# Kernel optimization log

Hardware: AMD Instinct MI355X
Metric: run time of the kernel (lower is better)

The kernel has to match this reference:

```python
import jax, jax.numpy as jnp
import numpy as np

N = 100_000      # nodes
E = 1_600_000    # edges (avg degree 16)
H = 2            # heads
C = 32           # out channels per head
L = 4            # EGAT layers
IN = 4           # input one-hot dim (node labels)
ECLS = 5         # edge classes (ratings)
SCALE = 0.1


def setup_inputs() -> dict:
    key = jax.random.key(0)
    ks = jax.random.split(key, 8)
    # node labels arange%4 -> equal user (0) / item (1) counts; x is one-hot (input_embedding=False)
    labels = jnp.arange(N) % 4
    x = jax.nn.one_hot(labels, IN, dtype=jnp.float32)
    edge_index = jax.random.randint(ks[0], (2, E), 0, N)
    edge_attr = jax.random.randint(ks[1], (E,), 0, ECLS)
    W0 = jax.random.normal(ks[2], (IN, H * C), dtype=jnp.float32) * SCALE
    W13 = jax.random.normal(ks[3], (L - 1, H * C, H * C), dtype=jnp.float32) * SCALE
    eemb = jax.random.normal(ks[4], (L, ECLS, H * C), dtype=jnp.float32) * SCALE
    att_src = jax.random.normal(ks[5], (L, H, C), dtype=jnp.float32) * SCALE
    att_dst = jax.random.normal(ks[6], (L, H, C), dtype=jnp.float32) * SCALE
    bias = jnp.zeros((L, H * C), dtype=jnp.float32)
    return dict(x=x, W0=W0, W13=W13, eemb=eemb, att_src=att_src,
                att_dst=att_dst, bias=bias, edge_index=edge_index, edge_attr=edge_attr)


def _egat_layer(x, W, eemb_l, a_src, a_dst, b, src, dst, edge_attr):
    # x: [N, Fin] -> h: [N, H, C]
    h = (x @ W).reshape(N, H, C)
    e = eemb_l[edge_attr].reshape(E, H, C)            # per-edge type embedding
    m = h[src] + e                                    # [E, H, C] edge-featured message
    logits = jax.nn.leaky_relu(
        jnp.sum(h[dst] * a_dst, axis=-1) + jnp.sum(m * a_src, axis=-1), 0.2)  # [E, H]
    # ragged softmax over incoming edges of each destination node
    amax = jax.ops.segment_max(logits, dst, num_segments=N)
    amax = jnp.where(jnp.isfinite(amax), amax, 0.0)
    ex = jnp.exp(logits - amax[dst])
    denom = jax.ops.segment_sum(ex, dst, num_segments=N)
    alpha = ex / (denom[dst] + 1e-16)                 # [E, H]
    out = jax.ops.segment_sum(alpha[..., None] * m, dst, num_segments=N)  # [N, H, C]
    return jax.nn.elu(out.reshape(N, H * C) + b)      # concat heads + elu activation


def reference(x, W0, W13, eemb, att_src, att_dst, bias, edge_index, edge_attr):
    src, dst = edge_index[0], edge_index[1]
    h = _egat_layer(x, W0, eemb[0], att_src[0], att_dst[0], bias[0], src, dst, edge_attr)
    for l in range(1, L):
        h = _egat_layer(h, W13[l - 1], eemb[l], att_src[l], att_dst[l], bias[l], src, dst, edge_attr)
    # users are nodes with label 0 (x[:,0]==1), items label 1 (x[:,1]==1);
    # labels were built as arange(N)%4, so user/item indices are static strided slices.
    user_idx = jnp.arange(0, N, 4)
    item_idx = jnp.arange(1, N, 4)
    u = h[user_idx]
    v = h[item_idx]
    return jnp.sum(u * v, axis=-1)  # MF decoder, multiply_by=1
```

## Files before the change

### kernel.cpp

```cpp
#include <hip/hip_runtime.h>
#include <hip/hip_bf16.h>
#include <math.h>

#define N_NODES 100000
#define N_EDGES 1600000
#define NPAIRS 25000
#define HC 64
#define NHEADS 2
#define NLAYERS 4
#define ECLS 5
#define NBUCK 196
#define NBLK 512
#define EPB (N_EDGES / NBLK)
#define NGRP (N_NODES / 16)
#define LIN0_BLOCKS 1024
#define FCAP 12288

typedef __attribute__((ext_vector_type(8))) short short8;
typedef __attribute__((ext_vector_type(4))) float floatx4;
union F8 { uint4 u; short8 s; };

__device__ inline float bf_lo(unsigned int u) { return __uint_as_float(u << 16); }
__device__ inline float bf_hi(unsigned int u) { return __uint_as_float(u & 0xffff0000u); }
__device__ inline unsigned short f2bf(float f) {
    unsigned int u = __float_as_uint(f);
    u += 0x7FFFu + ((u >> 16) & 1u);
    return (unsigned short)(u >> 16);
}

__global__ void k_chist_lin0(const int* __restrict__ dst, int* __restrict__ bh,
                             const float* __restrict__ in,
                             const float* __restrict__ W,
                             const float* __restrict__ asrc, const float* __restrict__ adst,
                             unsigned short* __restrict__ hcurb,
                             float* __restrict__ ssrc, float* __restrict__ sdst,
                             const float* __restrict__ eemb, float* __restrict__ escore) {
    int tid = threadIdx.x;
    if (blockIdx.x < NBLK) {
        __shared__ int lh[NBUCK];
        int blk = blockIdx.x;
        for (int i = tid; i < NBUCK; i += 256) lh[i] = 0;
        __syncthreads();
        int s = blk * EPB;
        for (int i = tid; i < EPB; i += 256) atomicAdd(&lh[dst[s + i] >> 9], 1);
        __syncthreads();
        for (int i = tid; i < NBUCK; i += 256) bh[i * NBLK + blk] = lh[i];
        return;
    }
    if (blockIdx.x >= NBLK + LIN0_BLOCKS) {
        if (tid < NLAYERS * ECLS * NHEADS) {
            int l = tid / (ECLS * NHEADS);
            int r = tid % (ECLS * NHEADS);
            int c = r >> 1;
            int h = r & 1;
            float s = 0.f;
            const float* ev = eemb + l * ECLS * HC + c * HC + h * 32;
            const float* av = asrc + l * HC + h * 32;
            for (int k = 0; k < 32; ++k) s += ev[k] * av[k];
            escore[tid] = s;
        }
        return;
    }
    int j = tid & 63;
    int wid = ((blockIdx.x - NBLK) * 256 + tid) >> 6;
    int nwaves = LIN0_BLOCKS * 4;

    float w0 = W[0 * HC + j], w1 = W[1 * HC + j], w2 = W[2 * HC + j], w3 = W[3 * HC + j];
    int head = j >> 5;
    int c = j & 31;
    float as = asrc[head * 32 + c];
    float ad = adst[head * 32 + c];

    for (int n = wid; n < N_NODES; n += nwaves) {
        int nu = __builtin_amdgcn_readfirstlane(n);
        float4 r = *(const float4*)(in + (size_t)nu * 4);
        float acc = r.x * w0 + r.y * w1 + r.z * w2 + r.w * w3;
        hcurb[(size_t)nu * HC + j] = f2bf(acc);
        float ps = acc * as;
        float pd = acc * ad;
        for (int off = 16; off > 0; off >>= 1) {
            ps += __shfl_down(ps, off, 32);
            pd += __shfl_down(pd, off, 32);
        }
        if (c == 0) {
            ssrc[nu * 2 + head] = ps;
            sdst[nu * 2 + head] = pd;
        }
    }
}

__global__ void k_s1(const int* __restrict__ bh, int* __restrict__ bbase,
                     int* __restrict__ part) {
    __shared__ int tmp[NBLK];
    int tid = threadIdx.x;
    int i = blockIdx.x * NBLK + tid;
    int v = bh[i];
    tmp[tid] = v;
    __syncthreads();
    for (int off = 1; off < NBLK; off <<= 1) {
        int t = (tid >= off) ? tmp[tid - off] : 0;
        __syncthreads();
        tmp[tid] += t;
        __syncthreads();
    }
    bbase[i] = tmp[tid] - v;
    if (tid == NBLK - 1) part[blockIdx.x] = tmp[NBLK - 1];
}

__global__ void k_cscatter(const int* __restrict__ src, const int* __restrict__ dst,
                           const int* __restrict__ attr, const int* __restrict__ bbase,
                           const int* __restrict__ part, int* __restrict__ bkt) {
    __shared__ int tmp[256];
    __shared__ int cur[NBUCK];
    __shared__ int gadj[NBUCK];
    __shared__ int stage[EPB];
    __shared__ unsigned char stb[EPB];
    int tid = threadIdx.x, blk = blockIdx.x;
    int pv = (tid < NBUCK) ? part[tid] : 0;
    tmp[tid] = pv;
    __syncthreads();
    for (int off = 1; off < 256; off <<= 1) {
        int t = (tid >= off) ? tmp[tid - off] : 0;
        __syncthreads();
        tmp[tid] += t;
        __syncthreads();
    }
    if (tid < NBUCK) gadj[tid] = tmp[tid] - pv;
    if (tid < NBUCK) cur[tid] = 0;
    for (int i = tid + 256; i < NBUCK; i += 256) cur[i] = 0;
    __syncthreads();
    int s0 = blk * EPB;
    for (int i = tid; i < EPB; i += 256) atomicAdd(&cur[dst[s0 + i] >> 9], 1);
    __syncthreads();
    int v = (tid < NBUCK) ? cur[tid] : 0;
    tmp[tid] = v;
    __syncthreads();
    for (int off = 1; off < 256; off <<= 1) {
        int t = (tid >= off) ? tmp[tid - off] : 0;
        __syncthreads();
        tmp[tid] += t;
        __syncthreads();
    }
    int ex = tmp[tid] - v;
    if (tid < NBUCK) {
        cur[tid] = ex;
        gadj[tid] += bbase[tid * NBLK + blk] - ex;
    }
    __syncthreads();
    for (int i = tid; i < EPB; i += 256) {
        int e = s0 + i;
        int d = dst[e];
        int b = d >> 9;
        int pos = atomicAdd(&cur[b], 1);
        stage[pos] = src[e] | (attr[e] << 17) | ((d & 511) << 20);
        stb[pos] = (unsigned char)b;
    }
    __syncthreads();
    for (int i = tid; i < EPB; i += 256)
        bkt[gadj[stb[i]] + i] = stage[i];
}

__global__ void k_fine(const int* __restrict__ part, const int* __restrict__ bkt,
                       int* __restrict__ packed, int* __restrict__ rowstart) {
    __shared__ int hist[512];
    __shared__ int cur[512];
    __shared__ int pscan[512];
    __shared__ int stage[FCAP];
    int b = blockIdx.x, tid = threadIdx.x;
    int pv = (tid < NBUCK) ? part[tid] : 0;
    pscan[tid] = pv;
    __syncthreads();
    for (int off = 1; off < 512; off <<= 1) {
        int t = (tid >= off) ? pscan[tid - off] : 0;
        __syncthreads();
        pscan[tid] += t;
        __syncthreads();
    }
    int base = (b == 0) ? 0 : pscan[b - 1];
    int bend = pscan[b];
    int nb = bend - base;
    hist[tid] = 0;
    __syncthreads();
    for (int i = tid; i < nb; i += 512)
        atomicAdd(&hist[(bkt[base + i] >> 20) & 0x1FF], 1);
    __syncthreads();
    int v = hist[tid];
    for (int off = 1; off < 512; off <<= 1) {
        int t = (tid >= off) ? hist[tid - off] : 0;
        __syncthreads();
        hist[tid] += t;
        __syncthreads();
    }
    int excl = hist[tid] - v;
    int node = (b << 9) + tid;
    if (node <= N_NODES) rowstart[node] = base + excl;
    cur[tid] = excl;
    __syncthreads();
    if (nb <= FCAP) {
        for (int i = tid; i < nb; i += 512) {
            int p = bkt[base + i];
            int r = atomicAdd(&cur[(p >> 20) & 0x1FF], 1);
            stage[r] = p;
        }
        __syncthreads();
        for (int i = tid; i < nb; i += 512) packed[base + i] = stage[i];
    } else {
        for (int i = tid; i < nb; i += 512) {
            int p = bkt[base + i];
            int r = atomicAdd(&cur[(p >> 20) & 0x1FF], 1);
            packed[base + r] = p;
        }
    }
}

__global__ void k_linmfma(const unsigned short* __restrict__ actB,
                          const float* __restrict__ Wl,
                          const float* __restrict__ asrc,
                          const float* __restrict__ adst,
                          unsigned short* __restrict__ hcurb,
                          float* __restrict__ ssrc, float* __restrict__ sdst) {
    __shared__ uint4 WB[512];
    __shared__ unsigned short Cb[4][1024];
    int tid = threadIdx.x;
    int lane = tid & 63;
    int w = tid >> 6;
    int q = lane >> 4;
    int c = lane & 15;

    for (int rid = tid; rid < 512; rid += 256) {
        int kk = rid >> 8;
        int t  = (rid >> 6) & 3;
        int ln = rid & 63;
        int qq = ln >> 4, cc = ln & 15;
        unsigned int u[4];
        #pragma unroll
        for (int jj = 0; jj < 4; ++jj) {
            float v0 = Wl[(kk * 32 + qq * 8 + jj * 2 + 0) * 64 + 16 * t + cc];
            float v1 = Wl[(kk * 32 + qq * 8 + jj * 2 + 1) * 64 + 16 * t + cc];
            u[jj] = (unsigned int)f2bf(v0) | ((unsigned int)f2bf(v1) << 16);
        }
        WB[rid] = make_uint4(u[0], u[1], u[2], u[3]);
    }
    __syncthreads();

    short8 bfr[2][4];
    #pragma unroll
    for (int kk = 0; kk < 2; ++kk)
        #pragma unroll
        for (int t = 0; t < 4; ++t) {
            F8 tmp; tmp.u = WB[(kk * 4 + t) * 64 + lane];
            bfr[kk][t] = tmp.s;
        }

    float as_[4], ad_[4];
    #pragma unroll
    for (int t = 0; t < 4; ++t) {
        as_[t] = asrc[16 * t + c];
        ad_[t] = adst[16 * t + c];
    }

    int wid = (blockIdx.x * 256 + tid) >> 6;
    int nwaves = gridDim.x * 4;

    for (int g = wid; g < NGRP; g += nwaves) {
        int base = g * 16;
        F8 a0, a1;
        a0.u = *(const uint4*)(actB + (size_t)(base + c) * HC + q * 8);
        a1.u = *(const uint4*)(actB + (size_t)(base + c) * HC + 32 + q * 8);

        floatx4 acc[4];
        #pragma unroll
        for (int t = 0; t < 4; ++t) {
            acc[t] = (floatx4){0.f, 0.f, 0.f, 0.f};
            acc[t] = __builtin_amdgcn_mfma_f32_16x16x32_bf16(a0.s, bfr[0][t], acc[t], 0, 0, 0);
            acc[t] = __builtin_amdgcn_mfma_f32_16x16x32_bf16(a1.s, bfr[1][t], acc[t], 0, 0, 0);
        }

        #pragma unroll
        for (int r = 0; r < 4; ++r) {
            float h0s = acc[0][r] * as_[0] + acc[1][r] * as_[1];
            float h1s = acc[2][r] * as_[2] + acc[3][r] * as_[3];
            float h0d = acc[0][r] * ad_[0] + acc[1][r] * ad_[1];
            float h1d = acc[2][r] * ad_[2] + acc[3][r] * ad_[3];
            #pragma unroll
            for (int off = 1; off < 16; off <<= 1) {
                h0s += __shfl_xor(h0s, off, 64);
                h1s += __shfl_xor(h1s, off, 64);
                h0d += __shfl_xor(h0d, off, 64);
                h1d += __shfl_xor(h1d, off, 64);
            }
            if (c == 0) {
                int node = base + q * 4 + r;
                *(float2*)(ssrc + node * 2) = make_float2(h0s, h1s);
                *(float2*)(sdst + node * 2) = make_float2(h0d, h1d);
            }
        }

        #pragma unroll
        for (int t = 0; t < 4; ++t)
            #pragma unroll
            for (int r = 0; r < 4; ++r)
                Cb[w][(q * 4 + r) * 64 + 16 * t + c] = f2bf(acc[t][r]);
        __builtin_amdgcn_wave_barrier();
        const uint4* cf = (const uint4*)&Cb[w][0];
        uint4* gout = (uint4*)(hcurb + (size_t)base * HC);
        gout[lane] = cf[lane];
        gout[64 + lane] = cf[64 + lane];
        __builtin_amdgcn_wave_barrier();
    }
}

template <bool LAST>
__global__ __launch_bounds__(256)
void k_edge2(const int* __restrict__ rowstart, const int* __restrict__ packed,
             const float* __restrict__ ssrc, const float* __restrict__ sdst,
             const float* __restrict__ escore_l,
             const unsigned short* __restrict__ hcurb,
             const float* __restrict__ eemb_l,
             const float* __restrict__ bias_l,
             unsigned short* __restrict__ actnext, float* __restrict__ out) {
    constexpr int SPAN = LAST ? 64 : 32;
    constexpr int CAP  = LAST ? 1440 : 800;
    __shared__ float4 ebuf[CAP];
    __shared__ float  cls[SPAN * 10];
    __shared__ float2 sdl[SPAN];
    __shared__ float2 esc2[ECLS];

    const int tid = threadIdx.x;
    const int n0 = blockIdx.x * SPAN;

    for (int i = tid; i < SPAN * 10; i += 256) cls[i] = 0.f;
    if (tid < ECLS) esc2[tid] = ((const float2*)escore_l)[tid];
    if (tid < SPAN) {
        int nn = n0 + tid; if (nn > N_NODES - 1) nn = N_NODES - 1;
        sdl[tid] = ((const float2*)sdst)[nn];
    }
    int spanEnd = n0 + SPAN; if (spanEnd > N_NODES) spanEnd = N_NODES;
    const int beg = rowstart[n0];
    const int end = rowstart[spanEnd];
    __syncthreads();

    const int nb = end - beg;
    for (int i = tid; i < nb; i += 256) {
        int p = packed[beg + i];
        int dl = ((p >> 20) & 511) - (n0 & 511);
        if (!LAST || ((dl & 2) == 0)) {
            int s = p & 0x1FFFF;
            int a = (p >> 17) & 7;
            float2 sv = *(const float2*)(ssrc + s * 2);
            float2 dv = sdl[dl];
            float2 ev = esc2[a];
            float l0 = dv.x + sv.x + ev.x; l0 = l0 >= 0.f ? l0 : 0.2f * l0;
            float l1 = dv.y + sv.y + ev.y; l1 = l1 >= 0.f ? l1 : 0.2f * l1;
            float w0 = __expf(l0), w1 = __expf(l1);
            if (i < CAP) ebuf[i] = make_float4(__int_as_float(p), w0, w1, 0.f);
            atomicAdd(&cls[dl * 10 + a * 2 + 0], w0);
            atomicAdd(&cls[dl * 10 + a * 2 + 1], w1);
        }
    }
    __syncthreads();

    const int lane = tid & 63;
    const int q = lane & 7;
    const int hh = q >> 2;
    const int slot = (tid >> 6) * 8 + (lane >> 3);
    int myn, pair = 0;
    bool valid = true;
    if (LAST) {
        pair = blockIdx.x * 16 + (slot >> 1);
        valid = pair < NPAIRS;
        myn = n0 + (slot >> 1) * 4 + (slot & 1);
    } else {
        myn = n0 + slot;
    }
    const int b0 = valid ? rowstart[myn] : 0;
    const int b1 = valid ? rowstart[myn + 1] : 0;
    const unsigned short* hb = hcurb + q * 8;

    float4 a0 = make_float4(0.f, 0.f, 0.f, 0.f);
    float4 a1 = make_float4(0.f, 0.f, 0.f, 0.f);

    struct PE { int p; float wt; };
    auto fetch = [&](int i) -> PE {
        PE r;
        int j = i - beg;
        if (j < CAP) {
            float4 t = ebuf[j];
            r.p = __float_as_int(t.x);
            r.wt = hh ? t.z : t.y;
        } else {
            int p = packed[i];
            int aa = (p >> 17) & 7;
            int ss = p & 0x1FFFF;
            int dll = ((p >> 20) & 511) - (n0 & 511);
            float2 dv2 = sdl[dll];
            float2 ev2 = esc2[aa];
            float lg = (hh ? dv2.y : dv2.x) + ssrc[ss * 2 + hh] + (hh ? ev2.y : ev2.x);
            lg = lg >= 0.f ? lg : 0.2f * lg;
            r.p = p;
            r.wt = __expf(lg);
        }
        return r;
    };

#define ACC8(wt, hv) do { \
        a0.x += (wt) * bf_lo((hv).x); a0.y += (wt) * bf_hi((hv).x); \
        a0.z += (wt) * bf_lo((hv).y); a0.w += (wt) * bf_hi((hv).y); \
        a1.x += (wt) * bf_lo((hv).z); a1.y += (wt) * bf_hi((hv).z); \
        a1.z += (wt) * bf_lo((hv).w); a1.w += (wt) * bf_hi((hv).w); \
    } while (0)

    int i = b0;
    for (; i + 2 <= b1; i += 2) {
        PE e0 = fetch(i);
        PE e1 = fetch(i + 1);
        uint4 h0 = *(const uint4*)(hb + ((e0.p & 0x1FFFF) << 6));
        uint4 h1 = *(const uint4*)(hb + ((e1.p & 0x1FFFF) << 6));
        ACC8(e0.wt, h0);
        ACC8(e1.wt, h1);
    }
    if (i < b1) {
        PE e0 = fetch(i);
        uint4 h0 = *(const uint4*)(hb + ((e0.p & 0x1FFFF) << 6));
        ACC8(e0.wt, h0);
    }
#undef ACC8

    const int dl = myn - n0;
    float ssum = 0.f;
    const float* ef = eemb_l + q * 8;
    #pragma unroll
    for (int a = 0; a < ECLS; ++a) {
        float c = cls[dl * 10 + a * 2 + hh];
        ssum += c;
        float4 e0 = *(const float4*)(ef + a * HC);
        float4 e1 = *(const float4*)(ef + a * HC + 4);
        a0.x += c * e0.x; a0.y += c * e0.y; a0.z += c * e0.z; a0.w += c * e0.w;
        a1.x += c * e1.x; a1.y += c * e1.y; a1.z += c * e1.z; a1.w += c * e1.w;
    }
    float inv = 1.f / (ssum + 1e-16f);
    float4 bv0 = *(const float4*)(bias_l + q * 8);
    float4 bv1 = *(const float4*)(bias_l + q * 8 + 4);
    float o0 = a0.x * inv + bv0.x; o0 = o0 > 0.f ? o0 : (__expf(o0) - 1.f);
    float o1 = a0.y * inv + bv0.y; o1 = o1 > 0.f ? o1 : (__expf(o1) - 1.f);
    float o2 = a0.z * inv + bv0.z; o2 = o2 > 0.f ? o2 : (__expf(o2) - 1.f);
    float o3 = a0.w * inv + bv0.w; o3 = o3 > 0.f ? o3 : (__expf(o3) - 1.f);
    float o4 = a1.x * inv + bv1.x; o4 = o4 > 0.f ? o4 : (__expf(o4) - 1.f);
    float o5 = a1.y * inv + bv1.y; o5 = o5 > 0.f ? o5 : (__expf(o5) - 1.f);
    float o6 = a1.z * inv + bv1.z; o6 = o6 > 0.f ? o6 : (__expf(o6) - 1.f);
    float o7 = a1.w * inv + bv1.w; o7 = o7 > 0.f ? o7 : (__expf(o7) - 1.f);

    if (!LAST) {
        unsigned int u0 = (unsigned int)f2bf(o0) | ((unsigned int)f2bf(o1) << 16);
        unsigned int u1 = (unsigned int)f2bf(o2) | ((unsigned int)f2bf(o3) << 16);
        unsigned int u2 = (unsigned int)f2bf(o4) | ((unsigned int)f2bf(o5) << 16);
        unsigned int u3 = (unsigned int)f2bf(o6) | ((unsigned int)f2bf(o7) << 16);
        *(uint4*)(actnext + (size_t)myn * HC + q * 8) = make_uint4(u0, u1, u2, u3);
    } else {
        float pdot = o0 * __shfl_xor(o0, 8, 64)
                   + o1 * __shfl_xor(o1, 8, 64)
                   + o2 * __shfl_xor(o2, 8, 64)
                   + o3 * __shfl_xor(o3, 8, 64)
                   + o4 * __shfl_xor(o4, 8, 64)
                   + o5 * __shfl_xor(o5, 8, 64)
                   + o6 * __shfl_xor(o6, 8, 64)
                   + o7 * __shfl_xor(o7, 8, 64);
        pdot += __shfl_xor(pdot, 1, 64);
        pdot += __shfl_xor(pdot, 2, 64);
        pdot += __shfl_xor(pdot, 4, 64);
        if (valid && ((slot & 1) == 0) && (q == 0)) out[pair] = pdot;
    }
}

extern "C" void kernel_launch(void* const* d_in, const int* in_sizes, int n_in,
                              void* d_out, int out_size, void* d_ws, size_t ws_size,
                              hipStream_t stream) {
    const float* x       = (const float*)d_in[0];
    const float* W0      = (const float*)d_in[1];
    const float* W13     = (const float*)d_in[2];
    const float* eemb    = (const float*)d_in[3];
    const float* att_src = (const float*)d_in[4];
    const float* att_dst = (const float*)d_in[5];
    const float* bias    = (const float*)d_in[6];
    const int*   eidx    = (const int*)d_in[7];
    const int*   eattr   = (const int*)d_in[8];
    float* out = (float*)d_out;

    const int* src = eidx;
    const int* dst = eidx + N_EDGES;

    char* wsb = (char*)d_ws;
    size_t off = 0;
    auto alloc = [&](size_t bytes) { char* p = wsb + off; off += (bytes + 255) & ~(size_t)255; return p; };
    unsigned short* hcurb  = (unsigned short*)alloc((size_t)N_NODES * HC * 2);
    unsigned short* actB   = (unsigned short*)alloc((size_t)N_NODES * HC * 2);
    float*          ssrc   = (float*)alloc((size_t)N_NODES * 2 * 4);
    float*          sdst   = (float*)alloc((size_t)N_NODES * 2 * 4);
    float*          escore = (float*)alloc(NLAYERS * ECLS * NHEADS * 4);
    int*            bh     = (int*)alloc((size_t)NBUCK * NBLK * 4);
    int*            bbase  = (int*)alloc((size_t)NBUCK * NBLK * 4);
    int*            part   = (int*)alloc(256 * 4);
    int*            rowstart = (int*)alloc(((size_t)N_NODES + 1) * 4);
    int*            bkt    = (int*)alloc((size_t)N_EDGES * 4);
    int*            packed = (int*)alloc((size_t)N_EDGES * 4);

    k_chist_lin0<<<NBLK + LIN0_BLOCKS + 1, 256, 0, stream>>>(
        dst, bh, x, W0, att_src, att_dst, hcurb, ssrc, sdst, eemb, escore);
    k_s1<<<NBUCK, NBLK, 0, stream>>>(bh, bbase, part);
    k_cscatter<<<NBLK, 256, 0, stream>>>(src, dst, eattr, bbase, part, bkt);
    k_fine<<<NBUCK, 512, 0, stream>>>(part, bkt, packed, rowstart);

    for (int l = 0; l < NLAYERS; ++l) {
        if (l > 0) {
            k_linmfma<<<512, 256, 0, stream>>>(
                actB, W13 + (size_t)(l - 1) * HC * HC,
                att_src + l * HC, att_dst + l * HC, hcurb, ssrc, sdst);
        }
        const float* esl = escore + l * ECLS * NHEADS;
        const float* el  = eemb + (size_t)l * ECLS * HC;
        const float* bl  = bias + l * HC;
        if (l < NLAYERS - 1)
            k_edge2<false><<<N_NODES / 32, 256, 0, stream>>>(
                rowstart, packed, ssrc, sdst, esl, hcurb, el, bl, actB, nullptr);
        else
            k_edge2<true><<<(NPAIRS + 15) / 16, 256, 0, stream>>>(
                rowstart, packed, ssrc, sdst, esl, hcurb, el, bl, nullptr, out);
    }
}
```

Baseline: 328.4 us.

## Widen edge aggregation blocks to 512 threads spanning 128 nodes with batched loads

```diff
diff --git a/kernel.cpp b/kernel.cpp
--- a/kernel.cpp
+++ b/kernel.cpp
@@ -20,6 +20,8 @@
 typedef __attribute__((ext_vector_type(4))) float floatx4;
 union F8 { uint4 u; short8 s; };
 
+struct PE { int p; float wt; };
+
 __device__ inline float bf_lo(unsigned int u) { return __uint_as_float(u << 16); }
 __device__ inline float bf_hi(unsigned int u) { return __uint_as_float(u & 0xffff0000u); }
 __device__ inline unsigned short f2bf(float f) {
@@ -127,7 +129,6 @@
     }
     if (tid < NBUCK) gadj[tid] = tmp[tid] - pv;
     if (tid < NBUCK) cur[tid] = 0;
-    for (int i = tid + 256; i < NBUCK; i += 256) cur[i] = 0;
     __syncthreads();
     int s0 = blk * EPB;
     for (int i = tid; i < EPB; i += 256) atomicAdd(&cur[dst[s0 + i] >> 9], 1);
@@ -311,17 +312,19 @@
 }
 
 template <bool LAST>
-__global__ __launch_bounds__(256)
-void k_edge2(const int* __restrict__ rowstart, const int* __restrict__ packed,
+__global__ __launch_bounds__(512)
+void k_edge4(const int* __restrict__ rowstart, const int* __restrict__ packed,
              const float* __restrict__ ssrc, const float* __restrict__ sdst,
              const float* __restrict__ escore_l,
              const unsigned short* __restrict__ hcurb,
              const float* __restrict__ eemb_l,
              const float* __restrict__ bias_l,
              unsigned short* __restrict__ actnext, float* __restrict__ out) {
-    constexpr int SPAN = LAST ? 64 : 32;
-    constexpr int CAP  = LAST ? 1440 : 800;
-    __shared__ float4 ebuf[CAP];
+    constexpr int SPAN = 128;
+    constexpr int CAP  = 2944;
+    __shared__ int   pe[CAP];
+    __shared__ float w0b[CAP];
+    __shared__ float w1b[CAP];
     __shared__ float  cls[SPAN * 10];
     __shared__ float2 sdl[SPAN];
     __shared__ float2 esc2[ECLS];
@@ -329,7 +332,7 @@
     const int tid = threadIdx.x;
     const int n0 = blockIdx.x * SPAN;
 
-    for (int i = tid; i < SPAN * 10; i += 256) cls[i] = 0.f;
+    for (int i = tid; i < SPAN * 10; i += 512) cls[i] = 0.f;
     if (tid < ECLS) esc2[tid] = ((const float2*)escore_l)[tid];
     if (tid < SPAN) {
         int nn = n0 + tid; if (nn > N_NODES - 1) nn = N_NODES - 1;
@@ -338,24 +341,37 @@
     int spanEnd = n0 + SPAN; if (spanEnd > N_NODES) spanEnd = N_NODES;
     const int beg = rowstart[n0];
     const int end = rowstart[spanEnd];
-    __syncthreads();
-
     const int nb = end - beg;
-    for (int i = tid; i < nb; i += 256) {
-        int p = packed[beg + i];
-        int dl = ((p >> 20) & 511) - (n0 & 511);
-        if (!LAST || ((dl & 2) == 0)) {
-            int s = p & 0x1FFFF;
-            int a = (p >> 17) & 7;
-            float2 sv = *(const float2*)(ssrc + s * 2);
-            float2 dv = sdl[dl];
+    __syncthreads();
+
+    for (int i0 = tid; i0 < nb; i0 += 2048) {
+        int pv[4]; bool act[4]; float2 sv[4]; int dl[4];
+        #pragma unroll
+        for (int k = 0; k < 4; ++k) {
+            int i = i0 + (k << 9);
+            act[k] = i < nb;
+            pv[k] = act[k] ? packed[beg + i] : 0;
+        }
+        #pragma unroll
+        for (int k = 0; k < 4; ++k) {
+            dl[k] = ((pv[k] >> 20) & 511) - (n0 & 511);
+            if (LAST) act[k] = act[k] && ((dl[k] & 2) == 0);
+            int s = pv[k] & 0x1FFFF;
+            sv[k] = act[k] ? *(const float2*)(ssrc + s * 2) : make_float2(0.f, 0.f);
+        }
+        #pragma unroll
+        for (int k = 0; k < 4; ++k) {
+            if (!act[k]) continue;
+            int i = i0 + (k << 9);
+            int a = (pv[k] >> 17) & 7;
+            float2 dv = sdl[dl[k]];
             float2 ev = esc2[a];
-            float l0 = dv.x + sv.x + ev.x; l0 = l0 >= 0.f ? l0 : 0.2f * l0;
-            float l1 = dv.y + sv.y + ev.y; l1 = l1 >= 0.f ? l1 : 0.2f * l1;
+            float l0 = dv.x + sv[k].x + ev.x; l0 = l0 >= 0.f ? l0 : 0.2f * l0;
+            float l1 = dv.y + sv[k].y + ev.y; l1 = l1 >= 0.f ? l1 : 0.2f * l1;
             float w0 = __expf(l0), w1 = __expf(l1);
-            if (i < CAP) ebuf[i] = make_float4(__int_as_float(p), w0, w1, 0.f);
-            atomicAdd(&cls[dl * 10 + a * 2 + 0], w0);
-            atomicAdd(&cls[dl * 10 + a * 2 + 1], w1);
+            if (i < CAP) { pe[i] = pv[k]; w0b[i] = w0; w1b[i] = w1; }
+            atomicAdd(&cls[dl[k] * 10 + a * 2 + 0], w0);
+            atomicAdd(&cls[dl[k] * 10 + a * 2 + 1], w1);
         }
     }
     __syncthreads();
@@ -364,111 +380,109 @@
     const int q = lane & 7;
     const int hh = q >> 2;
     const int slot = (tid >> 6) * 8 + (lane >> 3);
-    int myn, pair = 0;
-    bool valid = true;
-    if (LAST) {
-        pair = blockIdx.x * 16 + (slot >> 1);
-        valid = pair < NPAIRS;
-        myn = n0 + (slot >> 1) * 4 + (slot & 1);
-    } else {
-        myn = n0 + slot;
-    }
-    const int b0 = valid ? rowstart[myn] : 0;
-    const int b1 = valid ? rowstart[myn + 1] : 0;
     const unsigned short* hb = hcurb + q * 8;
 
-    float4 a0 = make_float4(0.f, 0.f, 0.f, 0.f);
-    float4 a1 = make_float4(0.f, 0.f, 0.f, 0.f);
-
-    struct PE { int p; float wt; };
-    auto fetch = [&](int i) -> PE {
-        PE r;
+    auto fetch = [&](int i, int dlc) -> PE {
         int j = i - beg;
         if (j < CAP) {
-            float4 t = ebuf[j];
-            r.p = __float_as_int(t.x);
-            r.wt = hh ? t.z : t.y;
-        } else {
-            int p = packed[i];
-            int aa = (p >> 17) & 7;
-            int ss = p & 0x1FFFF;
-            int dll = ((p >> 20) & 511) - (n0 & 511);
-            float2 dv2 = sdl[dll];
-            float2 ev2 = esc2[aa];
-            float lg = (hh ? dv2.y : dv2.x) + ssrc[ss * 2 + hh] + (hh ? ev2.y : ev2.x);
-            lg = lg >= 0.f ? lg : 0.2f * lg;
-            r.p = p;
-            r.wt = __expf(lg);
-        }
-        return r;
+            PE r; r.p = pe[j]; r.wt = hh ? w1b[j] : w0b[j]; return r;
+        }
+        int p = packed[i];
+        int a = (p >> 17) & 7;
+        int s = p & 0x1FFFF;
+        float2 dv2 = sdl[dlc];
+        float2 ev2 = esc2[a];
+        float lg = (hh ? dv2.y : dv2.x) + ssrc[s * 2 + hh] + (hh ? ev2.y : ev2.x);
+        lg = lg >= 0.f ? lg : 0.2f * lg;
+        PE r; r.p = p; r.wt = __expf(lg); return r;
     };
 
+    auto process_node = [&](int myn, float o[8]) {
+        const int dl = myn - n0;
+        const int b0 = rowstart[myn];
+        const int b1 = rowstart[myn + 1];
+        float4 a0 = make_float4(0.f, 0.f, 0.f, 0.f);
+        float4 a1 = make_float4(0.f, 0.f, 0.f, 0.f);
 #define ACC8(wt, hv) do { \
         a0.x += (wt) * bf_lo((hv).x); a0.y += (wt) * bf_hi((hv).x); \
         a0.z += (wt) * bf_lo((hv).y); a0.w += (wt) * bf_hi((hv).y); \
         a1.x += (wt) * bf_lo((hv).z); a1.y += (wt) * bf_hi((hv).z); \
         a1.z += (wt) * bf_lo((hv).w); a1.w += (wt) * bf_hi((hv).w); \
     } while (0)
-
-    int i = b0;
-    for (; i + 2 <= b1; i += 2) {
-        PE e0 = fetch(i);
-        PE e1 = fetch(i + 1);
-        uint4 h0 = *(const uint4*)(hb + ((e0.p & 0x1FFFF) << 6));
-        uint4 h1 = *(const uint4*)(hb + ((e1.p & 0x1FFFF) << 6));
-        ACC8(e0.wt, h0);
-        ACC8(e1.wt, h1);
-    }
-    if (i < b1) {
-        PE e0 = fetch(i);
-        uint4 h0 = *(const uint4*)(hb + ((e0.p & 0x1FFFF) << 6));
-        ACC8(e0.wt, h0);
-    }
+        int i = b0;
+        for (; i + 4 <= b1; i += 4) {
+            PE e0 = fetch(i, dl);
+            PE e1 = fetch(i + 1, dl);
+            PE e2 = fetch(i + 2, dl);
+            PE e3 = fetch(i + 3, dl);
+            uint4 h0 = *(const uint4*)(hb + (size_t)(e0.p & 0x1FFFF) * HC);
+            uint4 h1 = *(const uint4*)(hb + (size_t)(e1.p & 0x1FFFF) * HC);
+            uint4 h2 = *(const uint4*)(hb + (size_t)(e2.p & 0x1FFFF) * HC);
+            uint4 h3 = *(const uint4*)(hb + (size_t)(e3.p & 0x1FFFF) * HC);
+            ACC8(e0.wt, h0);
+            ACC8(e1.wt, h1);
+            ACC8(e2.wt, h2);
+            ACC8(e3.wt, h3);
+        }
+        for (; i < b1; ++i) {
+            PE e0 = fetch(i, dl);
+            uint4 h0 = *(const uint4*)(hb + (size_t)(e0.p & 0x1FFFF) * HC);
+            ACC8(e0.wt, h0);
+        }
 #undef ACC8
-
-    const int dl = myn - n0;
-    float ssum = 0.f;
-    const float* ef = eemb_l + q * 8;
-    #pragma unroll
-    for (int a = 0; a < ECLS; ++a) {
-        float c = cls[dl * 10 + a * 2 + hh];
-        ssum += c;
-        float4 e0 = *(const float4*)(ef + a * HC);
-        float4 e1 = *(const float4*)(ef + a * HC + 4);
-        a0.x += c * e0.x; a0.y += c * e0.y; a0.z += c * e0.z; a0.w += c * e0.w;
-        a1.x += c * e1.x; a1.y += c * e1.y; a1.z += c * e1.z; a1.w += c * e1.w;
-    }
-    float inv = 1.f / (ssum + 1e-16f);
-    float4 bv0 = *(const float4*)(bias_l + q * 8);
-    float4 bv1 = *(const float4*)(bias_l + q * 8 + 4);
-    float o0 = a0.x * inv + bv0.x; o0 = o0 > 0.f ? o0 : (__expf(o0) - 1.f);
-    float o1 = a0.y * inv + bv0.y; o1 = o1 > 0.f ? o1 : (__expf(o1) - 1.f);
-    float o2 = a0.z * inv + bv0.z; o2 = o2 > 0.f ? o2 : (__expf(o2) - 1.f);
-    float o3 = a0.w * inv + bv0.w; o3 = o3 > 0.f ? o3 : (__expf(o3) - 1.f);
-    float o4 = a1.x * inv + bv1.x; o4 = o4 > 0.f ? o4 : (__expf(o4) - 1.f);
-    float o5 = a1.y * inv + bv1.y; o5 = o5 > 0.f ? o5 : (__expf(o5) - 1.f);
-    float o6 = a1.z * inv + bv1.z; o6 = o6 > 0.f ? o6 : (__expf(o6) - 1.f);
-    float o7 = a1.w * inv + bv1.w; o7 = o7 > 0.f ? o7 : (__expf(o7) - 1.f);
+        float ssum = 0.f;
+        const float* ef = eemb_l + q * 8;
+        #pragma unroll
+        for (int a = 0; a < ECLS; ++a) {
+            float c = cls[dl * 10 + a * 2 + hh];
+            ssum += c;
+            float4 e0 = *(const float4*)(ef + a * HC);
+            float4 e1 = *(const float4*)(ef + a * HC + 4);
+            a0.x += c * e0.x; a0.y += c * e0.y; a0.z += c * e0.z; a0.w += c * e0.w;
+            a1.x += c * e1.x; a1.y += c * e1.y; a1.z += c * e1.z; a1.w += c * e1.w;
+        }
+        float inv = 1.f / (ssum + 1e-16f);
+        float4 bv0 = *(const float4*)(bias_l + q * 8);
+        float4 bv1 = *(const float4*)(bias_l + q * 8 + 4);
+        o[0] = a0.x * inv + bv0.x;
+        o[1] = a0.y * inv + bv0.y;
+        o[2] = a0.z * inv + bv0.z;
+        o[3] = a0.w * inv + bv0.w;
+        o[4] = a1.x * inv + bv1.x;
+        o[5] = a1.y * inv + bv1.y;
+        o[6] = a1.z * inv + bv1.z;
+        o[7] = a1.w * inv + bv1.w;
+        #pragma unroll
+        for (int k = 0; k < 8; ++k)
+            o[k] = o[k] > 0.f ? o[k] : (__expf(o[k]) - 1.f);
+    };
 
     if (!LAST) {
-        unsigned int u0 = (unsigned int)f2bf(o0) | ((unsigned int)f2bf(o1) << 16);
-        unsigned int u1 = (unsigned int)f2bf(o2) | ((unsigned int)f2bf(o3) << 16);
-        unsigned int u2 = (unsigned int)f2bf(o4) | ((unsigned int)f2bf(o5) << 16);
-        unsigned int u3 = (unsigned int)f2bf(o6) | ((unsigned int)f2bf(o7) << 16);
-        *(uint4*)(actnext + (size_t)myn * HC + q * 8) = make_uint4(u0, u1, u2, u3);
+        for (int nn = slot; nn < SPAN; nn += 64) {
+            int myn = n0 + nn;
+            if (myn >= N_NODES) break;
+            float o[8];
+            process_node(myn, o);
+            unsigned int u0 = (unsigned int)f2bf(o[0]) | ((unsigned int)f2bf(o[1]) << 16);
+            unsigned int u1 = (unsigned int)f2bf(o[2]) | ((unsigned int)f2bf(o[3]) << 16);
+            unsigned int u2 = (unsigned int)f2bf(o[4]) | ((unsigned int)f2bf(o[5]) << 16);
+            unsigned int u3 = (unsigned int)f2bf(o[6]) | ((unsigned int)f2bf(o[7]) << 16);
+            *(uint4*)(actnext + (size_t)myn * HC + q * 8) = make_uint4(u0, u1, u2, u3);
+        }
     } else {
-        float pdot = o0 * __shfl_xor(o0, 8, 64)
-                   + o1 * __shfl_xor(o1, 8, 64)
-                   + o2 * __shfl_xor(o2, 8, 64)
-                   + o3 * __shfl_xor(o3, 8, 64)
-                   + o4 * __shfl_xor(o4, 8, 64)
-                   + o5 * __shfl_xor(o5, 8, 64)
-                   + o6 * __shfl_xor(o6, 8, 64)
-                   + o7 * __shfl_xor(o7, 8, 64);
-        pdot += __shfl_xor(pdot, 1, 64);
-        pdot += __shfl_xor(pdot, 2, 64);
-        pdot += __shfl_xor(pdot, 4, 64);
-        if (valid && ((slot & 1) == 0) && (q == 0)) out[pair] = pdot;
+        int gp = blockIdx.x * 32 + (slot >> 1);
+        if (gp < NPAIRS) {
+            int myn = n0 + (slot >> 1) * 4 + (slot & 1);
+            float o[8];
+            process_node(myn, o);
+            float pd = 0.f;
+            #pragma unroll
+            for (int k = 0; k < 8; ++k) pd += o[k] * __shfl_xor(o[k], 8, 64);
+            pd += __shfl_xor(pd, 1, 64);
+            pd += __shfl_xor(pd, 2, 64);
+            pd += __shfl_xor(pd, 4, 64);
+            if (((slot & 1) == 0) && (q == 0)) out[gp] = pd;
+        }
     }
 }
 
@@ -510,6 +524,8 @@
     k_cscatter<<<NBLK, 256, 0, stream>>>(src, dst, eattr, bbase, part, bkt);
     k_fine<<<NBUCK, 512, 0, stream>>>(part, bkt, packed, rowstart);
 
+    const int EDGE_GRID = (N_NODES + 127) / 128;
+
     for (int l = 0; l < NLAYERS; ++l) {
         if (l > 0) {
             k_linmfma<<<512, 256, 0, stream>>>(
@@ -520,10 +536,10 @@
         const float* el  = eemb + (size_t)l * ECLS * HC;
         const float* bl  = bias + l * HC;
         if (l < NLAYERS - 1)
-            k_edge2<false><<<N_NODES / 32, 256, 0, stream>>>(
+            k_edge4<false><<<EDGE_GRID, 512, 0, stream>>>(
                 rowstart, packed, ssrc, sdst, esl, hcurb, el, bl, actB, nullptr);
         else
-            k_edge2<true><<<(NPAIRS + 15) / 16, 256, 0, stream>>>(
+            k_edge4<true><<<EDGE_GRID, 512, 0, stream>>>(
                 rowstart, packed, ssrc, sdst, esl, hcurb, el, bl, nullptr, out);
     }
 }
```

After: 367.6 us. 1.12x slower.
